# Kernel optimization log

Measured on AMD Instinct MI355X. Metric: run time of the kernel, lower is better.

## Reference

```python
import jax, jax.numpy as jnp
import numpy as np

EMB = 1024
HID = 4 * EMB
HEADS = 16
HEAD_DIM = EMB // HEADS


def gelu_tanh(x):
    c = jnp.sqrt(jnp.asarray(2.0 / jnp.pi, x.dtype))
    return 0.5 * x * (1.0 + jnp.tanh(c * (x + 0.044715 * x ** 3)))


def layernorm(x, scale, shift, eps=1e-5):
    mean = jnp.mean(x, axis=-1, keepdims=True)
    var = jnp.var(x, axis=-1, keepdims=True)
    return scale * (x - mean) / jnp.sqrt(var + eps) + shift


def setup_inputs() -> dict:
    key = jax.random.key(0)
    ks = jax.random.split(key, 12)
    s = 0.02
    return {
        "x": jax.random.normal(ks[0], (2, 2048, EMB), jnp.float32),
        "Wq": jax.random.normal(ks[1], (EMB, EMB), jnp.float32) * s,
        "Wk": jax.random.normal(ks[2], (EMB, EMB), jnp.float32) * s,
        "Wv": jax.random.normal(ks[3], (EMB, EMB), jnp.float32) * s,
        "Wo": jax.random.normal(ks[4], (EMB, EMB), jnp.float32) * s,
        "bo": jnp.zeros((EMB,), jnp.float32),
        "W1": jax.random.normal(ks[5], (EMB, HID), jnp.float32) * s,
        "b1": jnp.zeros((HID,), jnp.float32),
        "W2": jax.random.normal(ks[6], (HID, EMB), jnp.float32) * s,
        "b2": jnp.zeros((EMB,), jnp.float32),
        "ln1_scale": jnp.ones((EMB,), jnp.float32),
        "ln1_shift": jnp.zeros((EMB,), jnp.float32),
        "ln2_scale": jnp.ones((EMB,), jnp.float32),
        "ln2_shift": jnp.zeros((EMB,), jnp.float32),
    }


def reference(x, Wq, Wk, Wv, Wo, bo, W1, b1, W2, b2,
              ln1_scale, ln1_shift, ln2_scale, ln2_shift):
    B, S, D = x.shape

    # pre-norm attention + residual
    h = layernorm(x, ln1_scale, ln1_shift)
    q = (h @ Wq).reshape(B, S, HEADS, HEAD_DIM).transpose(0, 2, 1, 3)  # bhsd
    k = (h @ Wk).reshape(B, S, HEADS, HEAD_DIM).transpose(0, 2, 1, 3)
    v = (h @ Wv).reshape(B, S, HEADS, HEAD_DIM).transpose(0, 2, 1, 3)

    scores = jnp.einsum("bhqd,bhkd->bhqk", q, k)
    causal = jnp.tril(jnp.ones((S, S), bool))
    scores = jnp.where(causal, scores, -jnp.inf)
    attn = jax.nn.softmax(scores / jnp.sqrt(jnp.asarray(HEAD_DIM, x.dtype)), axis=-1)
    ctx = jnp.einsum("bhqk,bhkd->bhqd", attn, v)
    ctx = ctx.transpose(0, 2, 1, 3).reshape(B, S, D)
    x = x + (ctx @ Wo + bo)

    # pre-norm FFN + residual
    h = layernorm(x, ln2_scale, ln2_shift)
    h = gelu_tanh(h @ W1 + b1) @ W2 + b2
    return x + h
```

## Files before the change

### kernel.cpp

```cpp
#include <hip/hip_runtime.h>
#include <hip/hip_bf16.h>
#include <stdint.h>

#define B_   2
#define S_   2048
#define D_   1024
#define H_   16
#define DH_  64
#define HID_ 4096
#define M_   4096

typedef __bf16 bf16x8 __attribute__((ext_vector_type(8)));
typedef float  f32x4  __attribute__((ext_vector_type(4)));
typedef float  f32x16 __attribute__((ext_vector_type(16)));
typedef uint32_t u32x4v __attribute__((ext_vector_type(4)));

typedef const uint32_t __attribute__((address_space(1))) u32g;
typedef uint32_t       __attribute__((address_space(3))) u32l;

#define SCL2K_ 0.18033688011112042f

__device__ __forceinline__ uint16_t f2bf(float f) {
  uint32_t u = __builtin_bit_cast(uint32_t, f);
  u += 0x7FFFu + ((u >> 16) & 1u);
  return (uint16_t)(u >> 16);
}

__device__ __forceinline__ float bf2f(uint16_t u) {
  return __builtin_bit_cast(float, (uint32_t)u << 16);
}

__device__ __forceinline__ void gload_lds16(const void* g, void* l) {
  __builtin_amdgcn_global_load_lds((u32g*)g, (u32l*)l, 16, 0, 0);
}

__device__ __forceinline__ const bf16x8* lds8p(const uint16_t* base, int row,
                                               int cole) {
  int byt = (cole * 2) ^ ((row & 7) << 4);
  return reinterpret_cast<const bf16x8*>(base + row * 64 + (byt >> 1));
}

__device__ __forceinline__ uint32_t cvtpk_bf16(float lo, float hi) {
  uint32_t d;
  asm("v_cvt_pk_bf16_f32 %0, %1, %2" : "=v"(d) : "v"(lo), "v"(hi));
  return d;
}
__device__ __forceinline__ void pl32swap(uint32_t& a, uint32_t& b) {
  asm volatile("v_permlane32_swap_b32 %0, %1" : "+v"(a), "+v"(b));
}

__global__ void wconv_all(const float* __restrict__ Wq, const float* __restrict__ Wk,
                          const float* __restrict__ Wv, const float* __restrict__ Wo,
                          const float* __restrict__ W1, const float* __restrict__ W2,
                          uint16_t* __restrict__ WQKVT, uint16_t* __restrict__ WOT,
                          uint16_t* __restrict__ W1T, uint16_t* __restrict__ W2T) {
  __shared__ float tile[32][33];
  int idx = blockIdx.x;
  const float* W;
  uint16_t* WT;
  int K, N, within;
  if (idx < 4096) {
    int which = idx >> 10;
    within = idx & 1023;
    W = (which == 0) ? Wq : (which == 1) ? Wk : (which == 2) ? Wv : Wo;
    WT = (which == 3) ? WOT : WQKVT + (size_t)which * 1024 * 1024;
    K = 1024; N = 1024;
  } else if (idx < 8192) {
    within = idx - 4096; W = W1; WT = W1T; K = 1024; N = 4096;
  } else {
    within = idx - 8192; W = W2; WT = W2T; K = 4096; N = 1024;
  }
  int nb = N >> 5;
  int n0 = (within % nb) * 32, k0 = (within / nb) * 32;
  int tx = threadIdx.x, ty = threadIdx.y;
#pragma unroll
  for (int i = 0; i < 4; ++i)
    tile[ty + i * 8][tx] = W[(size_t)(k0 + ty + i * 8) * N + n0 + tx];
  __syncthreads();
#pragma unroll
  for (int i = 0; i < 4; ++i)
    WT[(size_t)(n0 + ty + i * 8) * K + k0 + tx] = f2bf(tile[tx][ty + i * 8]);
}

__global__ __launch_bounds__(256) void ln_k(const float* __restrict__ x,
                                            const float* __restrict__ sc,
                                            const float* __restrict__ sh,
                                            uint16_t* __restrict__ out) {
  int row = blockIdx.x;
  int t = threadIdx.x;
  float4 v = reinterpret_cast<const float4*>(x + (size_t)row * D_)[t];
  float s = v.x + v.y + v.z + v.w;
  float ss = v.x * v.x + v.y * v.y + v.z * v.z + v.w * v.w;
#pragma unroll
  for (int off = 32; off >= 1; off >>= 1) {
    s += __shfl_xor(s, off);
    ss += __shfl_xor(ss, off);
  }
  __shared__ float red[8];
  int wid = t >> 6, lane = t & 63;
  if (lane == 0) { red[wid] = s; red[wid + 4] = ss; }
  __syncthreads();
  s = red[0] + red[1] + red[2] + red[3];
  ss = red[4] + red[5] + red[6] + red[7];
  float mean = s * (1.0f / D_);
  float var = ss * (1.0f / D_) - mean * mean;
  float rstd = rsqrtf(var + 1e-5f);
  float4 g = reinterpret_cast<const float4*>(sc)[t];
  float4 b = reinterpret_cast<const float4*>(sh)[t];
  ushort4 o;
  o.x = f2bf(g.x * (v.x - mean) * rstd + b.x);
  o.y = f2bf(g.y * (v.y - mean) * rstd + b.y);
  o.z = f2bf(g.z * (v.z - mean) * rstd + b.z);
  o.w = f2bf(g.w * (v.w - mean) * rstd + b.w);
  reinterpret_cast<ushort4*>(out + (size_t)row * D_)[t] = o;
}

__global__ __launch_bounds__(256) void reduce4_k(
    const uint16_t* __restrict__ P0, const uint16_t* __restrict__ P1,
    const uint16_t* __restrict__ P2, const uint16_t* __restrict__ P3,
    const float* __restrict__ resid, const float* __restrict__ bias,
    float* __restrict__ out) {
  int row = blockIdx.x, t = threadIdx.x;
  size_t base = (size_t)row * D_ + t * 4;
  float4 r = *reinterpret_cast<const float4*>(resid + base);
  float4 b = reinterpret_cast<const float4*>(bias)[t];
  ushort4 u0 = *reinterpret_cast<const ushort4*>(P0 + base);
  ushort4 u1 = *reinterpret_cast<const ushort4*>(P1 + base);
  ushort4 u2 = *reinterpret_cast<const ushort4*>(P2 + base);
  ushort4 u3 = *reinterpret_cast<const ushort4*>(P3 + base);
  float4 o;
  o.x = r.x + b.x + bf2f(u0.x) + bf2f(u1.x) + bf2f(u2.x) + bf2f(u3.x);
  o.y = r.y + b.y + bf2f(u0.y) + bf2f(u1.y) + bf2f(u2.y) + bf2f(u3.y);
  o.z = r.z + b.z + bf2f(u0.z) + bf2f(u1.z) + bf2f(u2.z) + bf2f(u3.z);
  o.w = r.w + b.w + bf2f(u0.w) + bf2f(u1.w) + bf2f(u2.w) + bf2f(u3.w);
  *reinterpret_cast<float4*>(out + base) = o;
}

__global__ void vtrans_k(const uint16_t* __restrict__ V, uint16_t* __restrict__ VT) {
  __shared__ uint16_t tile[32][33];
  int s0 = blockIdx.x * 32, d0 = blockIdx.y * 32, bh = blockIdx.z;
  int tx = threadIdx.x, ty = threadIdx.y;
  const uint16_t* vb = V + (size_t)bh * S_ * DH_;
  uint16_t* vtb = VT + (size_t)bh * DH_ * S_;
#pragma unroll
  for (int i = 0; i < 4; ++i)
    tile[ty + i * 8][tx] = vb[(size_t)(s0 + ty + i * 8) * DH_ + d0 + tx];
  __syncthreads();
#pragma unroll
  for (int i = 0; i < 4; ++i)
    vtb[(size_t)(d0 + ty + i * 8) * S_ + s0 + tx] = tile[tx][ty + i * 8];
}

template <int EPI>
__global__ __launch_bounds__(512, 2) void gemm8(
    const uint16_t* __restrict__ A, const uint16_t* __restrict__ BT,
    void* __restrict__ Cout, const float* __restrict__ bias,
    uint16_t* __restrict__ P0, uint16_t* __restrict__ P1,
    uint16_t* __restrict__ P2, uint16_t* __restrict__ P3,
    int M, int N, int K) {
  __shared__ uint16_t As[2][2][128 * 64];
  __shared__ uint16_t Bs[2][2][128 * 64];
  int t = threadIdx.x;
  int lane = t & 63, wid = t >> 6;
  int wm = wid >> 2, wn = wid & 3;
  int l15 = lane & 15, lk8 = (lane >> 4) * 8, lr4 = (lane >> 4) * 4;
  int gx = gridDim.x;
  int nwg = gx * gridDim.y;
  int bid = blockIdx.y * gx + blockIdx.x;
  int swz = (bid & 7) * (nwg >> 3) + (bid >> 3);
  int bx = swz % gx, by = swz / gx;
  int m0 = by * 256, n0 = bx * 256;
  int ksz = K / gridDim.z;
  int kbeg = blockIdx.z * ksz;
  int NT = ksz >> 6;

  int r0 = t >> 3, slot0 = t & 7;
  int scol = (slot0 ^ (r0 & 7)) * 8;

  auto STAGE_A = [&](int kt, int half, int buf) {
    const uint16_t* src =
        A + (size_t)(m0 + half * 128 + r0) * K + kbeg + kt * 64 + scol;
    uint16_t* dst = &As[buf][half][t * 8];
    gload_lds16(src, dst);
    gload_lds16(src + (size_t)64 * K, dst + 4096);
  };
  auto STAGE_B = [&](int kt, int half, int buf) {
    const uint16_t* src =
        BT + (size_t)(n0 + half * 128 + r0) * K + kbeg + kt * 64 + scol;
    uint16_t* dst = &Bs[buf][half][t * 8];
    gload_lds16(src, dst);
    gload_lds16(src + (size_t)64 * K, dst + 4096);
  };

  bf16x8 a[4][2], b[2][2];
  auto LDA = [&](int buf, int mh) {
#pragma unroll
    for (int j = 0; j < 4; ++j)
#pragma unroll
      for (int kk = 0; kk < 2; ++kk)
        a[j][kk] = *lds8p(As[buf][mh], wm * 64 + j * 16 + l15, kk * 32 + lk8);
  };
  auto LDB = [&](int buf, int nh) {
#pragma unroll
    for (int jj = 0; jj < 2; ++jj)
#pragma unroll
      for (int kk = 0; kk < 2; ++kk)
        b[jj][kk] = *lds8p(Bs[buf][nh], wn * 32 + jj * 16 + l15, kk * 32 + lk8);
  };

  f32x4 acc[8][4] = {};
  auto MM = [&](int mh, int nh) {
    __builtin_amdgcn_s_setprio(1);
#pragma unroll
    for (int kk = 0; kk < 2; ++kk)
#pragma unroll
      for (int j = 0; j < 4; ++j)
#pragma unroll
        for (int jj = 0; jj < 2; ++jj)
          acc[mh * 4 + j][nh * 2 + jj] = __builtin_amdgcn_mfma_f32_16x16x32_bf16(
              a[j][kk], b[jj][kk], acc[mh * 4 + j][nh * 2 + jj], 0, 0, 0);
    __builtin_amdgcn_s_setprio(0);
  };
  auto BAR = [&]() {
    __builtin_amdgcn_s_barrier();
    asm volatile("" ::: "memory");
  };
  auto LGKM0 = [&]() {
    asm volatile("s_waitcnt lgkmcnt(0)" ::: "memory");
    __builtin_amdgcn_sched_barrier(0);
  };

  STAGE_A(0, 0, 0);
  STAGE_B(0, 1, 0);
  STAGE_B(0, 0, 0);
  STAGE_A(0, 1, 0);
  STAGE_A(1, 0, 1);
  STAGE_B(1, 1, 1);
  asm volatile("s_waitcnt vmcnt(4)" ::: "memory");
  BAR();

  for (int T = 0; T < NT; ++T) {
    int cur = T & 1;
    LDA(cur, 0);
    LDB(cur, 0);
    if (T + 1 < NT) STAGE_B(T + 1, 0, cur ^ 1);
    BAR(); LGKM0();
    MM(0, 0);
    BAR();
    LDB(cur, 1);
    if (T + 1 < NT) STAGE_A(T + 1, 1, cur ^ 1);
    BAR(); LGKM0();
    MM(0, 1);
    BAR();
    LDA(cur, 1);
    if (T + 2 < NT) STAGE_A(T + 2, 0, cur);
    BAR(); LGKM0();
    MM(1, 1);
    BAR();
    LDB(cur, 0);
    if (T + 2 < NT) STAGE_B(T + 2, 1, cur);
    BAR(); LGKM0();
    MM(1, 0);
    if (T + 1 < NT) {
      if (T == NT - 2) {
        asm volatile("s_waitcnt vmcnt(0)" ::: "memory");
      } else {
        asm volatile("s_waitcnt vmcnt(4)" ::: "memory");
      }
    }
    BAR();
  }

  uint16_t* Pz = nullptr;
  if constexpr (EPI == 3) {
    int z = blockIdx.z;
    Pz = (z == 0) ? P0 : (z == 1) ? P1 : (z == 2) ? P2 : P3;
  }
#pragma unroll
  for (int mi = 0; mi < 8; ++mi) {
#pragma unroll
    for (int ni = 0; ni < 4; ++ni) {
#pragma unroll
      for (int rr = 0; rr < 4; ++rr) {
        int gm = m0 + (mi >> 2) * 128 + wm * 64 + (mi & 3) * 16 + lr4 + rr;
        int gn = n0 + (ni >> 1) * 128 + wn * 32 + (ni & 1) * 16 + l15;
        float v = acc[mi][ni][rr];
        if constexpr (EPI == 0) {
          int which = gn >> 10, nc = gn & 1023;
          int h = nc >> 6, dh = nc & 63;
          int bb = gm >> 11, s = gm & 2047;
          if (which == 1) v *= SCL2K_;
          ((uint16_t*)Cout)[((size_t)which * 32 + bb * 16 + h) * (S_ * 64) +
                            (size_t)s * 64 + dh] = f2bf(v);
        } else if constexpr (EPI == 2) {
          float u = v + bias[gn];
          float y = 0.7978845608028654f * (u + 0.044715f * u * u * u);
          float e = __expf(2.0f * y);
          float th = 1.0f - 2.0f / (e + 1.0f);
          ((uint16_t*)Cout)[(size_t)gm * N + gn] = f2bf(0.5f * u * (1.0f + th));
        } else {
          Pz[(size_t)gm * N + gn] = f2bf(v);
        }
      }
    }
  }
}

template <int EPI>
__global__ __launch_bounds__(256) void gemm_bt(
    const uint16_t* __restrict__ A, const uint16_t* __restrict__ BT,
    void* __restrict__ Cout, const float* __restrict__ bias,
    const float* __restrict__ resid, int M, int N, int K) {
  __shared__ uint16_t Asm_[128 * 64];
  __shared__ uint16_t Bsm_[128 * 64];
  int t = threadIdx.x;
  int lane = t & 63, wid = t >> 6;
  int wr = wid >> 1, wc = wid & 1;
  int nwg = gridDim.x * gridDim.y;
  int bid = blockIdx.y * gridDim.x + blockIdx.x;
  int swz = (bid & 7) * (nwg >> 3) + (bid >> 3);
  int bx = swz % gridDim.x, by = swz / gridDim.x;
  int m0 = by * 128, n0 = bx * 128;
  int l15 = lane & 15, lk8 = (lane >> 4) * 8;
  f32x4 acc[4][4] = {};

  auto STAGE = [&](int k0) {
#pragma unroll
    for (int it = 0; it < 4; ++it) {
      int idx = it * 256 + t;
      int r = idx >> 3, slot = idx & 7;
      int c = (slot ^ (r & 7)) * 8;
      gload_lds16(A + (size_t)(m0 + r) * K + k0 + c, &Asm_[idx * 8]);
      gload_lds16(BT + (size_t)(n0 + r) * K + k0 + c, &Bsm_[idx * 8]);
    }
  };

  int niter = K >> 6;
  for (int ki = 0; ki < niter; ++ki) {
    __syncthreads();
    STAGE(ki * 64);
    __syncthreads();
#pragma unroll
    for (int kk = 0; kk < 2; ++kk) {
      bf16x8 a[4], b[4];
#pragma unroll
      for (int mi = 0; mi < 4; ++mi)
        a[mi] = *lds8p(Asm_, wr * 64 + mi * 16 + l15, kk * 32 + lk8);
#pragma unroll
      for (int ni = 0; ni < 4; ++ni)
        b[ni] = *lds8p(Bsm_, wc * 64 + ni * 16 + l15, kk * 32 + lk8);
#pragma unroll
      for (int mi = 0; mi < 4; ++mi)
#pragma unroll
        for (int ni = 0; ni < 4; ++ni)
          acc[mi][ni] = __builtin_amdgcn_mfma_f32_16x16x32_bf16(
              a[mi], b[ni], acc[mi][ni], 0, 0, 0);
    }
  }
  int lr4 = (lane >> 4) * 4;
#pragma unroll
  for (int mi = 0; mi < 4; ++mi) {
#pragma unroll
    for (int ni = 0; ni < 4; ++ni) {
#pragma unroll
      for (int r = 0; r < 4; ++r) {
        int gm = m0 + wr * 64 + mi * 16 + lr4 + r;
        int gn = n0 + wc * 64 + ni * 16 + l15;
        float v = acc[mi][ni][r];
        if constexpr (EPI == 1) {
          ((float*)Cout)[(size_t)gm * N + gn] =
              resid[(size_t)gm * N + gn] + v + bias[gn];
        }
      }
    }
  }
}

__global__ __launch_bounds__(64) void attn32s_k(const uint16_t* __restrict__ Q,
                                                const uint16_t* __restrict__ Kv,
                                                const uint16_t* __restrict__ VT,
                                                uint16_t* __restrict__ Obuf,
                                                float* __restrict__ ML) {
  int bid = blockIdx.x;
  int bh = bid & 31;
  int s = (bid >> 5) & 1;
  int qt = bid >> 6;
  int lane = threadIdx.x;
  int l31 = lane & 31, lh = lane >> 5;
  int nkt = qt + 1;
  int h = (nkt + 1) >> 1;
  int t0 = s ? h : 0, t1 = s ? nkt : h;
  int pb = ((qt * 32 + bh) << 1) + s;

  f32x16 o0 = {}, o1 = {};
  float mrow = -3.0e38f, lsum = 0.0f;

  const uint16_t* Kb = Kv + (size_t)bh * S_ * 64;
  const uint16_t* Vb = VT + (size_t)bh * 64 * S_;

  auto LOADKV = [&](int t, bf16x8 (&kf)[4], bf16x8 (&vf)[4]) {
    const uint16_t* kp = Kb + (size_t)(t * 32 + l31) * 64 + lh * 8;
#pragma unroll
    for (int dk = 0; dk < 4; ++dk)
      kf[dk] = *reinterpret_cast<const bf16x8*>(kp + dk * 16);
    const uint16_t* vp = Vb + (size_t)l31 * S_ + t * 32 + lh * 8;
    vf[0] = *reinterpret_cast<const bf16x8*>(vp);
    vf[1] = *reinterpret_cast<const bf16x8*>(vp + 16);
    vf[2] = *reinterpret_cast<const bf16x8*>(vp + 32 * S_);
    vf[3] = *reinterpret_cast<const bf16x8*>(vp + 32 * S_ + 16);
  };

  if (t0 < t1) {
    int qbase = qt * 32;
    bf16x8 qf[4];
#pragma unroll
    for (int dk = 0; dk < 4; ++dk)
      qf[dk] = *reinterpret_cast<const bf16x8*>(
          Q + ((size_t)bh * S_ + qbase + l31) * 64 + dk * 16 + lh * 8);

    auto COMPUTE = [&](int t, bf16x8 (&kf)[4], bf16x8 (&vf)[4]) {
      f32x16 Sf = {};
#pragma unroll
      for (int dk = 0; dk < 4; ++dk)
        Sf = __builtin_amdgcn_mfma_f32_32x32x16_bf16(kf[dk], qf[dk], Sf, 0, 0, 0);
      float sv[16];
      if (t == qt) {
#pragma unroll
        for (int rr = 0; rr < 16; ++rr) {
          int koff = (rr & 3) + 8 * (rr >> 2) + 4 * lh;
          sv[rr] = (koff <= l31) ? Sf[rr] : -3.0e38f;
        }
      } else {
#pragma unroll
        for (int rr = 0; rr < 16; ++rr) sv[rr] = Sf[rr];
      }
      float mt16 = sv[0];
#pragma unroll
      for (int rr = 1; rr < 16; ++rr) mt16 = fmaxf(mt16, sv[rr]);
      if (__any(mt16 > mrow + 8.0f)) {
        float mt = mt16;
#pragma unroll
        for (int off = 32; off >= 1; off >>= 1)
          mt = fmaxf(mt, __shfl_xor(mt, off));
        mt = fmaxf(mt, mrow);
        float fac = __builtin_amdgcn_exp2f(mrow - mt);
        mrow = mt;
        lsum *= fac;
#pragma unroll
        for (int rr = 0; rr < 16; ++rr) { o0[rr] *= fac; o1[rr] *= fac; }
      }
      float pv[16];
#pragma unroll
      for (int rr = 0; rr < 16; ++rr) {
        pv[rr] = __builtin_amdgcn_exp2f(sv[rr] - mrow);
        lsum += pv[rr];
      }
      uint32_t a0 = cvtpk_bf16(pv[0], pv[1]), b0 = cvtpk_bf16(pv[4], pv[5]);
      pl32swap(a0, b0);
      uint32_t a1 = cvtpk_bf16(pv[2], pv[3]), b1 = cvtpk_bf16(pv[6], pv[7]);
      pl32swap(a1, b1);
      u32x4v w0 = {a0, a1, b0, b1};
      bf16x8 pa0 = __builtin_bit_cast(bf16x8, w0);
      uint32_t a2 = cvtpk_bf16(pv[8], pv[9]), b2 = cvtpk_bf16(pv[12], pv[13]);
      pl32swap(a2, b2);
      uint32_t a3 = cvtpk_bf16(pv[10], pv[11]), b3 = cvtpk_bf16(pv[14], pv[15]);
      pl32swap(a3, b3);
      u32x4v w1 = {a2, a3, b2, b3};
      bf16x8 pa1 = __builtin_bit_cast(bf16x8, w1);
      o0 = __builtin_amdgcn_mfma_f32_32x32x16_bf16(pa0, vf[0], o0, 0, 0, 0);
      o0 = __builtin_amdgcn_mfma_f32_32x32x16_bf16(pa1, vf[1], o0, 0, 0, 0);
      o1 = __builtin_amdgcn_mfma_f32_32x32x16_bf16(pa0, vf[2], o1, 0, 0, 0);
      o1 = __builtin_amdgcn_mfma_f32_32x32x16_bf16(pa1, vf[3], o1, 0, 0, 0);
    };

    bf16x8 kA[4], vA[4], kB[4], vB[4];
    LOADKV(t0, kA, vA);
    int t = t0;
    while (t < t1) {
      if (t + 1 < t1) LOADKV(t + 1, kB, vB);
      COMPUTE(t, kA, vA);
      ++t;
      if (t >= t1) break;
      if (t + 1 < t1) LOADKV(t + 1, kA, vA);
      COMPUTE(t, kB, vB);
      ++t;
    }
    lsum += __shfl_xor(lsum, 32);
  }

  if (lane < 32) {
    ML[(size_t)pb * 64 + l31 * 2] = mrow;
    ML[(size_t)pb * 64 + l31 * 2 + 1] = lsum;
  }
#pragma unroll
  for (int rr = 0; rr < 16; ++rr) {
    int srow = (rr & 3) + 8 * (rr >> 2) + 4 * lh;
    size_t base = (size_t)pb * 2048 + srow * 64;
    Obuf[base + l31] = f2bf(o0[rr]);
    Obuf[base + 32 + l31] = f2bf(o1[rr]);
  }
}

__global__ __launch_bounds__(64) void attncomb_k(const uint16_t* __restrict__ Obuf,
                                                 const float* __restrict__ ML,
                                                 uint16_t* __restrict__ ctx) {
  int blk = blockIdx.x;
  int qt = blk >> 5, bh = blk & 31;
  int lane = threadIdx.x;
  int q = lane >> 1, half = lane & 1;
  size_t pb0 = (size_t)blk * 2, pb1 = pb0 + 1;
  float m0 = ML[pb0 * 64 + q * 2], l0 = ML[pb0 * 64 + q * 2 + 1];
  float m1 = ML[pb1 * 64 + q * 2], l1 = ML[pb1 * 64 + q * 2 + 1];
  float m = fmaxf(m0, m1);
  float w0 = __builtin_amdgcn_exp2f(m0 - m), w1 = __builtin_amdgcn_exp2f(m1 - m);
  float invL = 1.0f / (l0 * w0 + l1 * w1);
  int b_ = bh >> 4, h_ = bh & 15;
  int srow = qt * 32 + q;
  size_t ib = pb0 * 2048 + q * 64 + half * 32;
  size_t ob = ((size_t)(b_ * S_ + srow)) * D_ + h_ * 64 + half * 32;
#pragma unroll
  for (int i = 0; i < 8; ++i) {
    ushort4 u0 = *reinterpret_cast<const ushort4*>(Obuf + ib + i * 4);
    ushort4 u1 = *reinterpret_cast<const ushort4*>(Obuf + 2048 + ib + i * 4);
    ushort4 o;
    o.x = f2bf((bf2f(u0.x) * w0 + bf2f(u1.x) * w1) * invL);
    o.y = f2bf((bf2f(u0.y) * w0 + bf2f(u1.y) * w1) * invL);
    o.z = f2bf((bf2f(u0.z) * w0 + bf2f(u1.z) * w1) * invL);
    o.w = f2bf((bf2f(u0.w) * w0 + bf2f(u1.w) * w1) * invL);
    *reinterpret_cast<ushort4*>(ctx + ob + i * 4) = o;
  }
}

extern "C" void kernel_launch(void* const* d_in, const int* in_sizes, int n_in,
                              void* d_out, int out_size, void* d_ws, size_t ws_size,
                              hipStream_t stream) {
  const float* x    = (const float*)d_in[0];
  const float* Wq   = (const float*)d_in[1];
  const float* Wk   = (const float*)d_in[2];
  const float* Wv   = (const float*)d_in[3];
  const float* Wo   = (const float*)d_in[4];
  const float* bo   = (const float*)d_in[5];
  const float* W1   = (const float*)d_in[6];
  const float* b1   = (const float*)d_in[7];
  const float* W2   = (const float*)d_in[8];
  const float* b2   = (const float*)d_in[9];
  const float* ln1s = (const float*)d_in[10];
  const float* ln1b = (const float*)d_in[11];
  const float* ln2s = (const float*)d_in[12];
  const float* ln2b = (const float*)d_in[13];
  float* out = (float*)d_out;
  char* ws = (char*)d_ws;

  const size_t MB = 1024 * 1024;
  uint16_t* WQKVT = (uint16_t*)(ws + 0);
  uint16_t* WOT   = (uint16_t*)(ws + 6 * MB);
  uint16_t* W1T   = (uint16_t*)(ws + 8 * MB);
  uint16_t* W2T   = (uint16_t*)(ws + 16 * MB);
  uint16_t* H1    = (uint16_t*)(ws + 24 * MB);
  float*    X1    = (float*)(ws + 32 * MB);
  uint16_t* QKV   = (uint16_t*)(ws + 48 * MB);
  uint16_t* VTb   = (uint16_t*)(ws + 72 * MB);
  uint16_t* CTX   = (uint16_t*)(ws + 80 * MB);
  uint16_t* FFH   = (uint16_t*)(ws + 48 * MB);
  uint16_t* AOB   = (uint16_t*)(ws + 24 * MB);
  float*    AML   = (float*)(ws + 40 * MB);
  uint16_t* SP0   = (uint16_t*)(ws + 0);
  uint16_t* SP1   = (uint16_t*)(ws + 8 * MB);
  uint16_t* SP2   = (uint16_t*)(ws + 24 * MB);
  uint16_t* SP3   = (uint16_t*)(ws + 80 * MB);

  dim3 b32x8(32, 8);
  wconv_all<<<dim3(12288), b32x8, 0, stream>>>(Wq, Wk, Wv, Wo, W1, W2,
                                               WQKVT, WOT, W1T, W2T);
  ln_k<<<M_, 256, 0, stream>>>(x, ln1s, ln1b, H1);
  gemm8<0><<<dim3(12, 16), 512, 0, stream>>>(H1, WQKVT, QKV, nullptr,
                                             nullptr, nullptr, nullptr, nullptr,
                                             M_, 3072, 1024);
  const uint16_t* Qp = QKV;
  const uint16_t* Kp = QKV + (size_t)32 * S_ * 64;
  const uint16_t* Vp = QKV + (size_t)64 * S_ * 64;
  vtrans_k<<<dim3(64, 2, 32), b32x8, 0, stream>>>(Vp, VTb);
  attn32s_k<<<dim3(4096), 64, 0, stream>>>(Qp, Kp, VTb, AOB, AML);
  attncomb_k<<<dim3(2048), 64, 0, stream>>>(AOB, AML, CTX);
  gemm_bt<1><<<dim3(8, 32), 256, 0, stream>>>(CTX, WOT, X1, bo, x, M_, 1024, 1024);
  ln_k<<<M_, 256, 0, stream>>>(X1, ln2s, ln2b, H1);
  gemm8<2><<<dim3(16, 16), 512, 0, stream>>>(H1, W1T, FFH, b1,
                                             nullptr, nullptr, nullptr, nullptr,
                                             M_, 4096, 1024);
  gemm8<3><<<dim3(4, 16, 4), 512, 0, stream>>>(FFH, W2T, nullptr, nullptr,
                                               SP0, SP1, SP2, SP3,
                                               M_, 1024, 4096);
  reduce4_k<<<M_, 256, 0, stream>>>(SP0, SP1, SP2, SP3, X1, b2, out);
}
```

Baseline: 260.7 us.

## Stage attention K/V tiles through swizzled LDS with async global-to-LDS loads

The split-K attention kernel now loads each 32-key K and V^T tile into double-buffered shared memory with global_load_lds and an XOR swizzle, instead of loading them straight into registers. The loop waits on vmcnt to overlap the next tile's load with compute on the current one. MFMA operands are then read from LDS. This aims to cut register pressure and use wider, better-coalesced transfers. In exchange it adds LDS reads and manual waitcnt handling with a single 64-thread wave.

```diff
diff --git a/kernel.cpp b/kernel.cpp
--- a/kernel.cpp
+++ b/kernel.cpp
@@ -37,6 +37,12 @@
 __device__ __forceinline__ const bf16x8* lds8p(const uint16_t* base, int row,
                                                int cole) {
   int byt = (cole * 2) ^ ((row & 7) << 4);
+  return reinterpret_cast<const bf16x8*>(base + row * 64 + (byt >> 1));
+}
+
+__device__ __forceinline__ const bf16x8* lds8p32(const uint16_t* base, int row,
+                                                 int cole) {
+  int byt = (cole * 2) ^ ((row & 7) << 4) ^ ((row & 8) << 2);
   return reinterpret_cast<const bf16x8*>(base + row * 64 + (byt >> 1));
 }
 
@@ -381,6 +387,8 @@
                                                 const uint16_t* __restrict__ VT,
                                                 uint16_t* __restrict__ Obuf,
                                                 float* __restrict__ ML) {
+  __shared__ uint16_t Ksm[2][32 * 64];
+  __shared__ uint16_t Vsm[2][32 * 64];
   int bid = blockIdx.x;
   int bh = bid & 31;
   int s = (bid >> 5) & 1;
@@ -395,19 +403,18 @@
   f32x16 o0 = {}, o1 = {};
   float mrow = -3.0e38f, lsum = 0.0f;
 
-  const uint16_t* Kb = Kv + (size_t)bh * S_ * 64;
-  const uint16_t* Vb = VT + (size_t)bh * 64 * S_;
-
-  auto LOADKV = [&](int t, bf16x8 (&kf)[4], bf16x8 (&vf)[4]) {
-    const uint16_t* kp = Kb + (size_t)(t * 32 + l31) * 64 + lh * 8;
-#pragma unroll
-    for (int dk = 0; dk < 4; ++dk)
-      kf[dk] = *reinterpret_cast<const bf16x8*>(kp + dk * 16);
-    const uint16_t* vp = Vb + (size_t)l31 * S_ + t * 32 + lh * 8;
-    vf[0] = *reinterpret_cast<const bf16x8*>(vp);
-    vf[1] = *reinterpret_cast<const bf16x8*>(vp + 16);
-    vf[2] = *reinterpret_cast<const bf16x8*>(vp + 32 * S_);
-    vf[3] = *reinterpret_cast<const bf16x8*>(vp + 32 * S_ + 16);
+  auto STAGE = [&](int k0, int bufi) {
+#pragma unroll
+    for (int c = 0; c < 4; ++c) {
+      int idx = c * 64 + lane;
+      int r = idx >> 3, sl = idx & 7;
+      int slp = sl ^ (r & 7) ^ ((r & 8) >> 2);
+      gload_lds16(Kv + ((size_t)bh * S_ + k0 + r) * 64 + slp * 8,
+                  &Ksm[bufi][idx * 8]);
+      int dh = 2 * r + (slp >> 2), ko = (slp & 3) * 8;
+      gload_lds16(VT + ((size_t)bh * 64 + dh) * S_ + k0 + ko,
+                  &Vsm[bufi][idx * 8]);
+    }
   };
 
   if (t0 < t1) {
@@ -418,11 +425,22 @@
       qf[dk] = *reinterpret_cast<const bf16x8*>(
           Q + ((size_t)bh * S_ + qbase + l31) * 64 + dk * 16 + lh * 8);
 
-    auto COMPUTE = [&](int t, bf16x8 (&kf)[4], bf16x8 (&vf)[4]) {
+    int buf = 0;
+    STAGE(t0 * 32, 0);
+    for (int t = t0; t < t1; ++t) {
+      if (t + 1 < t1) {
+        STAGE((t + 1) * 32, buf ^ 1);
+        asm volatile("s_waitcnt vmcnt(8)" ::: "memory");
+      } else {
+        asm volatile("s_waitcnt vmcnt(0)" ::: "memory");
+      }
+      __builtin_amdgcn_sched_barrier(0);
       f32x16 Sf = {};
 #pragma unroll
-      for (int dk = 0; dk < 4; ++dk)
-        Sf = __builtin_amdgcn_mfma_f32_32x32x16_bf16(kf[dk], qf[dk], Sf, 0, 0, 0);
+      for (int dk = 0; dk < 4; ++dk) {
+        bf16x8 kf = *lds8p32(Ksm[buf], l31, dk * 16 + lh * 8);
+        Sf = __builtin_amdgcn_mfma_f32_32x32x16_bf16(kf, qf[dk], Sf, 0, 0, 0);
+      }
       float sv[16];
       if (t == qt) {
 #pragma unroll
@@ -467,23 +485,16 @@
       pl32swap(a3, b3);
       u32x4v w1 = {a2, a3, b2, b3};
       bf16x8 pa1 = __builtin_bit_cast(bf16x8, w1);
-      o0 = __builtin_amdgcn_mfma_f32_32x32x16_bf16(pa0, vf[0], o0, 0, 0, 0);
-      o0 = __builtin_amdgcn_mfma_f32_32x32x16_bf16(pa1, vf[1], o0, 0, 0, 0);
-      o1 = __builtin_amdgcn_mfma_f32_32x32x16_bf16(pa0, vf[2], o1, 0, 0, 0);
-      o1 = __builtin_amdgcn_mfma_f32_32x32x16_bf16(pa1, vf[3], o1, 0, 0, 0);
-    };
-
-    bf16x8 kA[4], vA[4], kB[4], vB[4];
-    LOADKV(t0, kA, vA);
-    int t = t0;
-    while (t < t1) {
-      if (t + 1 < t1) LOADKV(t + 1, kB, vB);
-      COMPUTE(t, kA, vA);
-      ++t;
-      if (t >= t1) break;
-      if (t + 1 < t1) LOADKV(t + 1, kA, vA);
-      COMPUTE(t, kB, vB);
-      ++t;
+      int vrow = l31 >> 1, vcb = (l31 & 1) * 32 + lh * 8;
+      bf16x8 v00 = *lds8p32(Vsm[buf], vrow, vcb);
+      o0 = __builtin_amdgcn_mfma_f32_32x32x16_bf16(pa0, v00, o0, 0, 0, 0);
+      bf16x8 v01 = *lds8p32(Vsm[buf], vrow, vcb + 16);
+      o0 = __builtin_amdgcn_mfma_f32_32x32x16_bf16(pa1, v01, o0, 0, 0, 0);
+      bf16x8 v10 = *lds8p32(Vsm[buf], 16 + vrow, vcb);
+      o1 = __builtin_amdgcn_mfma_f32_32x32x16_bf16(pa0, v10, o1, 0, 0, 0);
+      bf16x8 v11 = *lds8p32(Vsm[buf], 16 + vrow, vcb + 16);
+      o1 = __builtin_amdgcn_mfma_f32_32x32x16_bf16(pa1, v11, o1, 0, 0, 0);
+      buf ^= 1;
     }
     lsum += __shfl_xor(lsum, 32);
   }
```

New measurement: 245.8 us. -5.7%, faster.
